# Optimization experiments

Measured on AMD Instinct MI355X. Metric: run time of the kernel, lower is better.

## Reference

```python
import jax, jax.numpy as jnp
import numpy as np

B, N_CAPS, N_VOTES, D_IN, D_H, D_CP = 1024, 64, 36, 256, 128, 32
TWO_PI = 2.0 * np.pi


def geometric_transform(pose):
    # pose: [..., 6] -> affine 3x3 matrix [..., 3, 3] (nonlinear, full affine)
    sx, sy, theta, shear, tx, ty = jnp.split(pose, 6, axis=-1)
    sx = jax.nn.sigmoid(sx) + 1e-2
    sy = jax.nn.sigmoid(sy) + 1e-2
    tx = jnp.tanh(tx * 5.0)
    ty = jnp.tanh(ty * 5.0)
    shear = jnp.tanh(shear * 5.0)
    theta = theta * TWO_PI
    c, s = jnp.cos(theta), jnp.sin(theta)
    row0 = jnp.concatenate([sx * c + shear * sy * s, -sx * s + shear * sy * c, tx], -1)
    row1 = jnp.concatenate([sy * s, sy * c, ty], -1)
    zeros = jnp.zeros_like(tx)
    row2 = jnp.concatenate([zeros, zeros, jnp.ones_like(tx)], -1)
    return jnp.stack([row0, row1, row2], axis=-2)


def setup_inputs() -> dict:
    key = jax.random.key(0)
    ks = jax.random.split(key, 16)
    u = lambda k, shp: 0.5 * (jax.random.uniform(k, shp, jnp.float32) - 0.5)
    return {
        "features": jax.random.normal(ks[0], (B, N_CAPS, D_IN), jnp.float32),
        "w1": u(ks[1], (1, N_CAPS, D_IN, D_H)),
        "b1": jnp.zeros((1, N_CAPS, 1, D_H), jnp.float32),
        "w2": u(ks[2], (1, N_CAPS, D_H, D_CP)),
        "b2": jnp.zeros((1, N_CAPS, 1, D_CP), jnp.float32),
        "caps_mlp_w": u(ks[3], (1, N_CAPS, D_CP + 1, D_H)),
        "caps_mlp_b": jnp.zeros((1, N_CAPS, 1, D_H), jnp.float32),
        "cpr_dynamic_w": u(ks[4], (1, N_CAPS, D_H, N_VOTES * 6)),
        "ccr_w": u(ks[5], (1, N_CAPS, D_H, 6)),
        "ccr_b": jnp.zeros((1, N_CAPS, 1, 6), jnp.float32),
        "pres_caps_w": u(ks[6], (1, N_CAPS, D_H, 1)),
        "pres_caps_b": jnp.zeros((1, N_CAPS, 1, 1), jnp.float32),
        "pres_vote_w": u(ks[7], (1, N_CAPS, D_H, N_VOTES)),
        "pres_vote_b": jnp.zeros((1, N_CAPS, 1, N_VOTES), jnp.float32),
        "scale_vote_w": u(ks[8], (1, N_CAPS, D_H, N_VOTES)),
        "scale_vote_b": jnp.zeros((1, N_CAPS, 1, N_VOTES), jnp.float32),
        "cpr_static": jax.random.uniform(ks[9], (1, N_CAPS, N_VOTES, 6), jnp.float32) - 0.5,
    }


def reference(features, w1, b1, w2, b2, caps_mlp_w, caps_mlp_b, cpr_dynamic_w,
              ccr_w, ccr_b, pres_caps_w, pres_caps_b, pres_vote_w, pres_vote_b,
              scale_vote_w, scale_vote_b, cpr_static):
    batch_size = features.shape[0]
    x = features[:, :, None, :]                               # [B, C, 1, 256]
    h = jax.nn.relu(x @ w1 + b1)                              # [B, C, 1, H]
    raw_caps_params = jax.nn.relu(h @ w2 + b2)                # [B, C, 1, P]
    caps_exist = jnp.ones(raw_caps_params.shape[:-1] + (1,), raw_caps_params.dtype)
    caps_params = jnp.concatenate([raw_caps_params, caps_exist], -1)  # [B, C, 1, P+1]
    caps_feat = jax.nn.relu(caps_params @ caps_mlp_w + caps_mlp_b)    # [B, C, 1, H]

    cpr_dynamic = (caps_feat @ cpr_dynamic_w).reshape(batch_size, N_CAPS, N_VOTES, 6)
    ccr = caps_feat @ ccr_w + ccr_b                           # [B, C, 1, 6]
    pres_logit_per_caps = (caps_feat @ pres_caps_w + pres_caps_b)[:, :, 0, :]   # [B, C, 1]
    pres_logit_per_vote = (caps_feat @ pres_vote_w + pres_vote_b)[:, :, 0, :]   # [B, C, V]
    scale_per_vote = (caps_feat @ scale_vote_w + scale_vote_b)[:, :, 0, :]      # [B, C, V]

    ccr_mat = geometric_transform(ccr)                        # [B, C, 1, 3, 3]
    cpr_mat = geometric_transform(cpr_dynamic + cpr_static)   # [B, C, V, 3, 3]
    votes = ccr_mat @ cpr_mat                                 # [B, C, V, 3, 3]

    pres_per_caps = jax.nn.sigmoid(pres_logit_per_caps)
    pres_per_vote = pres_per_caps * jax.nn.sigmoid(pres_logit_per_vote)
    scale_per_vote = jax.nn.softplus(scale_per_vote + 0.5) + 0.01
    dynamic_weights_l2 = jnp.sum(cpr_dynamic ** 2) / batch_size / 2.0
    return (votes, scale_per_vote, pres_per_vote, pres_logit_per_caps,
            pres_logit_per_vote, dynamic_weights_l2, raw_caps_params[:, :, 0, :], features)
```

## Files before the change

kernel.cpp:

```cpp
#include <hip/hip_runtime.h>
#include <math.h>

#define NB   1024
#define NC   64
#define DIN  256
#define DH   128
#define DCP  32
#define NV   36

#define OFF0 0
#define OFF1 21233664
#define OFF2 23592960
#define OFF3 25952256
#define OFF4 26017792
#define OFF5 28377088
#define OFF6 28377089
#define OFF7 30474241

#define SM_FST 0
#define SM_R2  4224
#define SM_R3  8576
#define SM_TOT 9664

#define SM_XS  SM_R2
#define SM_W1C (SM_R2 + 544)
#define SM_W2S SM_R2
#define SM_WM  SM_R2
#define SM_WH  SM_R2
#define SM_HD  (SM_R2 + 1280)
#define SM_HB  (SM_R2 + 3872)
#define SM_WD  SM_R2
#define SM_DYN SM_R2
#define SM_CPS SM_R3
#define SM_M   SM_R3
#define SM_PSIG (SM_R3 + 192)

__device__ __forceinline__ float sigm(float x) { return 1.0f / (1.0f + __expf(-x)); }
__device__ __forceinline__ float tanh5(float x) {
    x = fminf(fmaxf(5.0f * x, -15.0f), 15.0f);
    float z = __expf(2.0f * x);
    return (z - 1.0f) / (z + 1.0f);
}
__device__ __forceinline__ void geo(const float* p, float* m) {
    float sx = sigm(p[0]) + 0.01f;
    float sy = sigm(p[1]) + 0.01f;
    float th = p[2] * 6.28318530717958647692f;
    float sh = tanh5(p[3]);
    float tx = tanh5(p[4]);
    float ty = tanh5(p[5]);
    float cc = __cosf(th), ss = __sinf(th);
    m[0] =  sx * cc + sh * sy * ss;
    m[1] = -sx * ss + sh * sy * cc;
    m[2] = tx;
    m[3] = sy * ss;
    m[4] = sy * cc;
    m[5] = ty;
}

__global__ void zero_l2_kernel(float* out) { out[OFF5] = 0.0f; }

__global__ __launch_bounds__(256, 4)
void caps_fused_kernel(const float* __restrict__ feat,
                       const float* __restrict__ w1,  const float* __restrict__ b1,
                       const float* __restrict__ w2,  const float* __restrict__ b2,
                       const float* __restrict__ wm,  const float* __restrict__ bm,
                       const float* __restrict__ wdy,
                       const float* __restrict__ wccr,const float* __restrict__ bccr,
                       const float* __restrict__ wpc, const float* __restrict__ bpc,
                       const float* __restrict__ wpv, const float* __restrict__ bpv,
                       const float* __restrict__ wsv, const float* __restrict__ bsv,
                       const float* __restrict__ cst,
                       float* __restrict__ out)
{
    __shared__ float sm[SM_TOT];
    const int t  = threadIdx.x;
    const int c  = blockIdx.y;
    const int rb = blockIdx.x * 32;

    {
        const int tx = t & 31;
        const int ty = t >> 5;
        float acc[4][4] = {};
        const int xrow = t >> 3, xk2 = (t & 7) * 2;
        for (int k0 = 0; k0 < DIN; k0 += 16) {
            __syncthreads();
            {
                const int gi = (rb + xrow) * (NC * DIN) + c * DIN + k0 + xk2;
                const float2 v = *(const float2*)&feat[gi];
                sm[SM_XS + xrow * 17 + xk2]     = v.x;
                sm[SM_XS + xrow * 17 + xk2 + 1] = v.y;
                out[OFF7 + gi]     = v.x;
                out[OFF7 + gi + 1] = v.y;
            }
            *(float4*)&sm[SM_W1C + t * 4] =
                *(const float4*)&w1[c * (DIN * DH) + k0 * DH + t * 4];
            *(float4*)&sm[SM_W1C + (t + 256) * 4] =
                *(const float4*)&w1[c * (DIN * DH) + k0 * DH + (t + 256) * 4];
            __syncthreads();
#pragma unroll
            for (int kk = 0; kk < 16; ++kk) {
                const float a0 = sm[SM_XS + (ty * 4 + 0) * 17 + kk];
                const float a1 = sm[SM_XS + (ty * 4 + 1) * 17 + kk];
                const float a2 = sm[SM_XS + (ty * 4 + 2) * 17 + kk];
                const float a3 = sm[SM_XS + (ty * 4 + 3) * 17 + kk];
                const float4 bv = *(const float4*)&sm[SM_W1C + kk * DH + tx * 4];
                acc[0][0] += a0 * bv.x; acc[0][1] += a0 * bv.y; acc[0][2] += a0 * bv.z; acc[0][3] += a0 * bv.w;
                acc[1][0] += a1 * bv.x; acc[1][1] += a1 * bv.y; acc[1][2] += a1 * bv.z; acc[1][3] += a1 * bv.w;
                acc[2][0] += a2 * bv.x; acc[2][1] += a2 * bv.y; acc[2][2] += a2 * bv.z; acc[2][3] += a2 * bv.w;
                acc[3][0] += a3 * bv.x; acc[3][1] += a3 * bv.y; acc[3][2] += a3 * bv.z; acc[3][3] += a3 * bv.w;
            }
        }
        const float4 bb4 = *(const float4*)&b1[c * DH + tx * 4];
        const float bb[4] = { bb4.x, bb4.y, bb4.z, bb4.w };
#pragma unroll
        for (int i = 0; i < 4; ++i)
#pragma unroll
            for (int j = 0; j < 4; ++j) {
                float v = fmaxf(acc[i][j] + bb[j], 0.0f);
                sm[SM_FST + (tx * 4 + j) * 33 + (ty * 4 + i)] = v;
            }
    }
    __syncthreads();

#pragma unroll
    for (int p = 0; p < 4; ++p) {
        const int idx = t + p * 256;
        *(float4*)&sm[SM_W2S + idx * 4] = *(const float4*)&w2[c * (DH * DCP) + idx * 4];
    }
    __syncthreads();
    {
        const int b  = t & 31;
        const int j4 = (t >> 5) << 2;
        float acc[4] = {};
#pragma unroll 8
        for (int k = 0; k < DH; ++k) {
            const float h = sm[SM_FST + k * 33 + b];
            const float4 wv = *(const float4*)&sm[SM_W2S + k * DCP + j4];
            acc[0] += h * wv.x; acc[1] += h * wv.y; acc[2] += h * wv.z; acc[3] += h * wv.w;
        }
#pragma unroll
        for (int jj = 0; jj < 4; ++jj) {
            const float v = fmaxf(acc[jj] + b2[c * DCP + j4 + jj], 0.0f);
            out[OFF6 + ((rb + b) * NC + c) * DCP + j4 + jj] = v;
            sm[SM_CPS + b * 34 + j4 + jj] = v;
        }
        if (t < 32) sm[SM_CPS + t * 34 + 32] = 1.0f;
    }
    __syncthreads();

#pragma unroll
    for (int p = 0; p < 5; ++p) {
        const int idx = t + p * 256;
        if (idx < 1056)
            *(float4*)&sm[SM_WM + idx * 4] = *(const float4*)&wm[c * (33 * DH) + idx * 4];
    }
    __syncthreads();
    {
        const int b  = t & 31;
        const int nb = (t >> 5) << 4;
        float acc[16] = {};
        for (int k = 0; k < 33; ++k) {
            const float a = sm[SM_CPS + b * 34 + k];
#pragma unroll
            for (int jq = 0; jq < 4; ++jq) {
                const float4 wv = *(const float4*)&sm[SM_WM + k * DH + nb + jq * 4];
                acc[jq*4+0] += a * wv.x; acc[jq*4+1] += a * wv.y;
                acc[jq*4+2] += a * wv.z; acc[jq*4+3] += a * wv.w;
            }
        }
#pragma unroll
        for (int j = 0; j < 16; ++j) {
            const float v = fmaxf(acc[j] + bm[c * DH + nb + j], 0.0f);
            sm[SM_FST + (nb + j) * 33 + b] = v;
        }
    }
    __syncthreads();

    {
        const int txx = t & 15;
        const int tyy = t >> 4;
        float acc[2][5] = {};
        for (int k0 = 0; k0 < DH; k0 += 16) {
            __syncthreads();
#pragma unroll
            for (int p = 0; p < 5; ++p) {
                const int idx = t + p * 256;
                const int kk = idx / 80, col = idx % 80;
                const int kg = k0 + kk;
                float v = 0.0f;
                if (col < 6)        v = wccr[c * (DH * 6) + kg * 6 + col];
                else if (col == 6)  v = wpc[c * DH + kg];
                else if (col < 43)  v = wpv[c * (DH * NV) + kg * NV + (col - 7)];
                else if (col < 79)  v = wsv[c * (DH * NV) + kg * NV + (col - 43)];
                sm[SM_WH + kk * 80 + col] = v;
            }
            if (k0 == 0 && t < 80) {
                float v = 0.0f;
                if (t < 6)       v = bccr[c * 6 + t];
                else if (t == 6) v = bpc[c];
                else if (t < 43) v = bpv[c * NV + (t - 7)];
                else if (t < 79) v = bsv[c * NV + (t - 43)];
                sm[SM_HB + t] = v;
            }
            __syncthreads();
#pragma unroll
            for (int kk = 0; kk < 16; ++kk) {
                const float a0 = sm[SM_FST + (k0 + kk) * 33 + tyy * 2 + 0];
                const float a1 = sm[SM_FST + (k0 + kk) * 33 + tyy * 2 + 1];
#pragma unroll
                for (int j = 0; j < 5; ++j) {
                    const float w = sm[SM_WH + kk * 80 + txx * 5 + j];
                    acc[0][j] += a0 * w;
                    acc[1][j] += a1 * w;
                }
            }
        }
#pragma unroll
        for (int i = 0; i < 2; ++i)
#pragma unroll
            for (int j = 0; j < 5; ++j)
                sm[SM_HD + (tyy * 2 + i) * 81 + txx * 5 + j] = acc[i][j];
    }
    __syncthreads();

    if (t < 32) {
        const int b = t;
        const float plc = sm[SM_HD + b * 81 + 6] + sm[SM_HB + 6];
        out[OFF3 + (rb + b) * NC + c] = plc;
        sm[SM_PSIG + b] = sigm(plc);
        float p[6], m[6];
#pragma unroll
        for (int i = 0; i < 6; ++i) p[i] = sm[SM_HD + b * 81 + i] + sm[SM_HB + i];
        geo(p, m);
#pragma unroll
        for (int i = 0; i < 6; ++i) sm[SM_M + b * 6 + i] = m[i];
    }
    __syncthreads();

#pragma unroll
    for (int p = 0; p < 10; ++p) {
        const int item = t + p * 256;
        const int b = item / 80, col = item % 80;
        if (col >= 7 && col < 79) {
            const float v = sm[SM_HD + b * 81 + col] + sm[SM_HB + col];
            const int base = ((rb + b) * NC + c) * NV;
            if (col < 43) {
                const int o = col - 7;
                out[OFF4 + base + o] = v;
                out[OFF2 + base + o] = sm[SM_PSIG + b] * sigm(v);
            } else {
                const int o = col - 43;
                float sp = v + 0.5f;
                sp = (sp > 15.0f) ? sp : log1pf(__expf(sp));
                out[OFF1 + base + o] = sp + 0.01f;
            }
        }
    }

    float l2loc = 0.0f;
    {
        const int g   = t & 63;
        const int ty4 = t >> 6;
        float acc[8][4] = {};
        for (int k0 = 0; k0 < DH; k0 += 16) {
            __syncthreads();
#pragma unroll
            for (int p = 0; p < 7; ++p) {
                const int i2  = t + p * 256;
                const int col = (i2 * 2) % 224;
                const int row = (i2 * 2) / 224;
                float2 v = make_float2(0.0f, 0.0f);
                if (col < 216)
                    v = *(const float2*)&wdy[c * (DH * 216) + (k0 + row) * 216 + col];
                *(float2*)&sm[SM_WD + row * 224 + col] = v;
            }
            __syncthreads();
#pragma unroll
            for (int kk = 0; kk < 16; ++kk) {
                float a[8];
#pragma unroll
                for (int i = 0; i < 8; ++i)
                    a[i] = sm[SM_FST + (k0 + kk) * 33 + ty4 * 8 + i];
                const float4 w = *(const float4*)&sm[SM_WD + kk * 224 + g * 4];
#pragma unroll
                for (int i = 0; i < 8; ++i) {
                    acc[i][0] += a[i] * w.x; acc[i][1] += a[i] * w.y;
                    acc[i][2] += a[i] * w.z; acc[i][3] += a[i] * w.w;
                }
            }
        }
        for (int half = 0; half < 2; ++half) {
            __syncthreads();
            if (g < 54 && (g >= 27) == (half == 1)) {
#pragma unroll
                for (int i = 0; i < 8; ++i)
#pragma unroll
                    for (int j = 0; j < 4; ++j)
                        sm[SM_DYN + (ty4 * 8 + i) * 109 + (g * 4 + j - half * 108)] = acc[i][j];
            }
            __syncthreads();
#pragma unroll
            for (int p = 0; p < 3; ++p) {
                const int item = t + p * 256;
                if (item < 576) {
                    const int b = item / 18, vh = item % 18;
                    const int v = half * 18 + vh;
                    float dyn[6], pose[6], mB[6];
                    float ss = 0.0f;
#pragma unroll
                    for (int j = 0; j < 6; ++j) {
                        dyn[j] = sm[SM_DYN + b * 109 + vh * 6 + j];
                        ss += dyn[j] * dyn[j];
                        pose[j] = dyn[j] + cst[c * (NV * 6) + v * 6 + j];
                    }
                    l2loc += ss;
                    geo(pose, mB);
                    const float A0 = sm[SM_M + b * 6 + 0], A1 = sm[SM_M + b * 6 + 1];
                    const float A2 = sm[SM_M + b * 6 + 2], A3 = sm[SM_M + b * 6 + 3];
                    const float A4 = sm[SM_M + b * 6 + 4], A5 = sm[SM_M + b * 6 + 5];
                    const int ob = (((rb + b) * NC + c) * NV + v) * 9;
                    out[OFF0 + ob + 0] = A0 * mB[0] + A1 * mB[3];
                    out[OFF0 + ob + 1] = A0 * mB[1] + A1 * mB[4];
                    out[OFF0 + ob + 2] = A0 * mB[2] + A1 * mB[5] + A2;
                    out[OFF0 + ob + 3] = A3 * mB[0] + A4 * mB[3];
                    out[OFF0 + ob + 4] = A3 * mB[1] + A4 * mB[4];
                    out[OFF0 + ob + 5] = A3 * mB[2] + A4 * mB[5] + A5;
                    out[OFF0 + ob + 6] = 0.0f;
                    out[OFF0 + ob + 7] = 0.0f;
                    out[OFF0 + ob + 8] = 1.0f;
                }
            }
        }
    }

    l2loc += __shfl_down(l2loc, 32, 64);
    l2loc += __shfl_down(l2loc, 16, 64);
    l2loc += __shfl_down(l2loc, 8, 64);
    l2loc += __shfl_down(l2loc, 4, 64);
    l2loc += __shfl_down(l2loc, 2, 64);
    l2loc += __shfl_down(l2loc, 1, 64);
    if ((t & 63) == 0) atomicAdd(&out[OFF5], l2loc * (1.0f / 2048.0f));
}

extern "C" void kernel_launch(void* const* d_in, const int* in_sizes, int n_in,
                              void* d_out, int out_size, void* d_ws, size_t ws_size,
                              hipStream_t stream)
{
    const float* feat = (const float*)d_in[0];
    const float* w1   = (const float*)d_in[1];
    const float* b1   = (const float*)d_in[2];
    const float* w2   = (const float*)d_in[3];
    const float* b2   = (const float*)d_in[4];
    const float* wm   = (const float*)d_in[5];
    const float* bm   = (const float*)d_in[6];
    const float* wdy  = (const float*)d_in[7];
    const float* wccr = (const float*)d_in[8];
    const float* bccr = (const float*)d_in[9];
    const float* wpc  = (const float*)d_in[10];
    const float* bpc  = (const float*)d_in[11];
    const float* wpv  = (const float*)d_in[12];
    const float* bpv  = (const float*)d_in[13];
    const float* wsv  = (const float*)d_in[14];
    const float* bsv  = (const float*)d_in[15];
    const float* cst  = (const float*)d_in[16];
    float* out = (float*)d_out;

    zero_l2_kernel<<<1, 1, 0, stream>>>(out);
    dim3 grid(NB / 32, NC);
    caps_fused_kernel<<<grid, 256, 0, stream>>>(feat, w1, b1, w2, b2, wm, bm, wdy,
                                                wccr, bccr, wpc, bpc, wpv, bpv,
                                                wsv, bsv, cst, out);
}
```

Baseline: 624.8 us.

## Register-prefetch global tiles, pad shared strides for vector loads, offload feature copy

Adds register double-buffering: the next k-tile of w1/features, the w2 and wm tiles, the head weights and the wdy tiles are loaded into registers while the current tile is computed. Shared-memory row strides change from 33/34 to 36 so activations can be read as float4/float2. The constant-one column of the caps MLP is folded into a separate bias add. The features passthrough copy moves out of the kernel into a device-to-device hipMemcpyAsync. The aim is to hide global load latency and cut shared-memory instruction count. The cost is higher register pressure under launch_bounds(256,4), possible bank conflicts from the new stride, and a separate memcpy pass over the features.

```diff
diff --git a/kernel.cpp b/kernel.cpp
--- a/kernel.cpp
+++ b/kernel.cpp
@@ -18,12 +18,12 @@
 #define OFF7 30474241
 
 #define SM_FST 0
-#define SM_R2  4224
-#define SM_R3  8576
-#define SM_TOT 9664
+#define SM_R2  4608
+#define SM_R3  8960
+#define SM_TOT 10112
 
 #define SM_XS  SM_R2
-#define SM_W1C (SM_R2 + 544)
+#define SM_W1C (SM_R2 + 576)
 #define SM_W2S SM_R2
 #define SM_WM  SM_R2
 #define SM_WH  SM_R2
@@ -76,105 +76,155 @@
     const int t  = threadIdx.x;
     const int c  = blockIdx.y;
     const int rb = blockIdx.x * 32;
+    const int t4 = t * 4;
+
+    float4 w2pf[4];
 
     {
         const int tx = t & 31;
         const int ty = t >> 5;
+        const int xrow = t >> 3, xk2 = (t & 7) * 2;
+        const float* fsrc = &feat[(rb + xrow) * (NC * DIN) + c * DIN + xk2];
+        const float* w1b_ = &w1[c * (DIN * DH)];
+        float2 xr  = *(const float2*)fsrc;
+        float4 wra = *(const float4*)(w1b_ + t4);
+        float4 wrb = *(const float4*)(w1b_ + 1024 + t4);
         float acc[4][4] = {};
-        const int xrow = t >> 3, xk2 = (t & 7) * 2;
         for (int k0 = 0; k0 < DIN; k0 += 16) {
             __syncthreads();
-            {
-                const int gi = (rb + xrow) * (NC * DIN) + c * DIN + k0 + xk2;
-                const float2 v = *(const float2*)&feat[gi];
-                sm[SM_XS + xrow * 17 + xk2]     = v.x;
-                sm[SM_XS + xrow * 17 + xk2 + 1] = v.y;
-                out[OFF7 + gi]     = v.x;
-                out[OFF7 + gi + 1] = v.y;
-            }
-            *(float4*)&sm[SM_W1C + t * 4] =
-                *(const float4*)&w1[c * (DIN * DH) + k0 * DH + t * 4];
-            *(float4*)&sm[SM_W1C + (t + 256) * 4] =
-                *(const float4*)&w1[c * (DIN * DH) + k0 * DH + (t + 256) * 4];
-            __syncthreads();
+            sm[SM_XS + xk2 * 36 + xrow]       = xr.x;
+            sm[SM_XS + (xk2 + 1) * 36 + xrow] = xr.y;
+            *(float4*)&sm[SM_W1C + t4]        = wra;
+            *(float4*)&sm[SM_W1C + 1024 + t4] = wrb;
+            __syncthreads();
+            if (k0 + 16 < DIN) {
+                xr  = *(const float2*)(fsrc + k0 + 16);
+                wra = *(const float4*)(w1b_ + (k0 + 16) * DH + t4);
+                wrb = *(const float4*)(w1b_ + (k0 + 16) * DH + 1024 + t4);
+            } else {
+#pragma unroll
+                for (int p = 0; p < 4; ++p)
+                    w2pf[p] = *(const float4*)&w2[c * (DH * DCP) + (t + p * 256) * 4];
+            }
 #pragma unroll
             for (int kk = 0; kk < 16; ++kk) {
-                const float a0 = sm[SM_XS + (ty * 4 + 0) * 17 + kk];
-                const float a1 = sm[SM_XS + (ty * 4 + 1) * 17 + kk];
-                const float a2 = sm[SM_XS + (ty * 4 + 2) * 17 + kk];
-                const float a3 = sm[SM_XS + (ty * 4 + 3) * 17 + kk];
+                const float4 av = *(const float4*)&sm[SM_XS + kk * 36 + ty * 4];
                 const float4 bv = *(const float4*)&sm[SM_W1C + kk * DH + tx * 4];
-                acc[0][0] += a0 * bv.x; acc[0][1] += a0 * bv.y; acc[0][2] += a0 * bv.z; acc[0][3] += a0 * bv.w;
-                acc[1][0] += a1 * bv.x; acc[1][1] += a1 * bv.y; acc[1][2] += a1 * bv.z; acc[1][3] += a1 * bv.w;
-                acc[2][0] += a2 * bv.x; acc[2][1] += a2 * bv.y; acc[2][2] += a2 * bv.z; acc[2][3] += a2 * bv.w;
-                acc[3][0] += a3 * bv.x; acc[3][1] += a3 * bv.y; acc[3][2] += a3 * bv.z; acc[3][3] += a3 * bv.w;
-            }
-        }
-        const float4 bb4 = *(const float4*)&b1[c * DH + tx * 4];
-        const float bb[4] = { bb4.x, bb4.y, bb4.z, bb4.w };
-#pragma unroll
-        for (int i = 0; i < 4; ++i)
-#pragma unroll
-            for (int j = 0; j < 4; ++j) {
-                float v = fmaxf(acc[i][j] + bb[j], 0.0f);
-                sm[SM_FST + (tx * 4 + j) * 33 + (ty * 4 + i)] = v;
-            }
-    }
-    __syncthreads();
-
-#pragma unroll
-    for (int p = 0; p < 4; ++p) {
-        const int idx = t + p * 256;
-        *(float4*)&sm[SM_W2S + idx * 4] = *(const float4*)&w2[c * (DH * DCP) + idx * 4];
-    }
-    __syncthreads();
-    {
+                acc[0][0] += av.x * bv.x; acc[0][1] += av.x * bv.y; acc[0][2] += av.x * bv.z; acc[0][3] += av.x * bv.w;
+                acc[1][0] += av.y * bv.x; acc[1][1] += av.y * bv.y; acc[1][2] += av.y * bv.z; acc[1][3] += av.y * bv.w;
+                acc[2][0] += av.z * bv.x; acc[2][1] += av.z * bv.y; acc[2][2] += av.z * bv.z; acc[2][3] += av.z * bv.w;
+                acc[3][0] += av.w * bv.x; acc[3][1] += av.w * bv.y; acc[3][2] += av.w * bv.z; acc[3][3] += av.w * bv.w;
+            }
+        }
+        const float4 bb = *(const float4*)&b1[c * DH + tx * 4];
+        const float bbA[4] = { bb.x, bb.y, bb.z, bb.w };
+#pragma unroll
+        for (int j = 0; j < 4; ++j) {
+            float4 vv;
+            vv.x = fmaxf(acc[0][j] + bbA[j], 0.0f);
+            vv.y = fmaxf(acc[1][j] + bbA[j], 0.0f);
+            vv.z = fmaxf(acc[2][j] + bbA[j], 0.0f);
+            vv.w = fmaxf(acc[3][j] + bbA[j], 0.0f);
+            *(float4*)&sm[SM_FST + (tx * 4 + j) * 36 + ty * 4] = vv;
+        }
+    }
+
+    __syncthreads();
+#pragma unroll
+    for (int p = 0; p < 4; ++p)
+        *(float4*)&sm[SM_W2S + t4 + p * 1024] = w2pf[p];
+    __syncthreads();
+    float4 wmpf[5];
+    {
+#pragma unroll
+        for (int p = 0; p < 5; ++p) {
+            const int idx = t + p * 256;
+            if (idx < 1056)
+                wmpf[p] = *(const float4*)&wm[c * (33 * DH) + idx * 4];
+        }
         const int b  = t & 31;
         const int j4 = (t >> 5) << 2;
         float acc[4] = {};
 #pragma unroll 8
         for (int k = 0; k < DH; ++k) {
-            const float h = sm[SM_FST + k * 33 + b];
+            const float h = sm[SM_FST + k * 36 + b];
             const float4 wv = *(const float4*)&sm[SM_W2S + k * DCP + j4];
             acc[0] += h * wv.x; acc[1] += h * wv.y; acc[2] += h * wv.z; acc[3] += h * wv.w;
         }
+        const float4 b2v = *(const float4*)&b2[c * DCP + j4];
+        const float b2A[4] = { b2v.x, b2v.y, b2v.z, b2v.w };
 #pragma unroll
         for (int jj = 0; jj < 4; ++jj) {
-            const float v = fmaxf(acc[jj] + b2[c * DCP + j4 + jj], 0.0f);
+            const float v = fmaxf(acc[jj] + b2A[jj], 0.0f);
             out[OFF6 + ((rb + b) * NC + c) * DCP + j4 + jj] = v;
-            sm[SM_CPS + b * 34 + j4 + jj] = v;
-        }
-        if (t < 32) sm[SM_CPS + t * 34 + 32] = 1.0f;
-    }
-    __syncthreads();
-
+            sm[SM_CPS + b * 36 + j4 + jj] = v;
+        }
+    }
+
+    __syncthreads();
 #pragma unroll
     for (int p = 0; p < 5; ++p) {
         const int idx = t + p * 256;
         if (idx < 1056)
-            *(float4*)&sm[SM_WM + idx * 4] = *(const float4*)&wm[c * (33 * DH) + idx * 4];
-    }
-    __syncthreads();
+            *(float4*)&sm[SM_WM + idx * 4] = wmpf[p];
+    }
+    __syncthreads();
+    const float* d2p[5]; int d2adv[5]; float d2msk[5], d2pf[5];
+#pragma unroll
+    for (int p = 0; p < 5; ++p) {
+        const int idx = t + p * 256;
+        const int kp = idx / 80, colp = idx - kp * 80;
+        const float* s; int st; float mk = 1.0f;
+        if (colp < 6)       { s = &wccr[c * (DH * 6) + kp * 6 + colp];          st = 6;  }
+        else if (colp == 6) { s = &wpc [c * DH + kp];                            st = 1;  }
+        else if (colp < 43) { s = &wpv [c * (DH * NV) + kp * NV + (colp - 7)];   st = NV; }
+        else if (colp < 79) { s = &wsv [c * (DH * NV) + kp * NV + (colp - 43)];  st = NV; }
+        else                { s = &wccr[c * (DH * 6)]; st = 0; mk = 0.0f; }
+        d2pf[p]  = *s;
+        d2p[p]   = s + st * 16;
+        d2adv[p] = st * 16;
+        d2msk[p] = mk;
+    }
+    float bpf = 0.0f;
+    if (t < 80) {
+        if (t < 6)       bpf = bccr[c * 6 + t];
+        else if (t == 6) bpf = bpc[c];
+        else if (t < 43) bpf = bpv[c * NV + (t - 7)];
+        else if (t < 79) bpf = bsv[c * NV + (t - 43)];
+    }
     {
         const int b  = t & 31;
         const int nb = (t >> 5) << 4;
         float acc[16] = {};
-        for (int k = 0; k < 33; ++k) {
-            const float a = sm[SM_CPS + b * 34 + k];
-#pragma unroll
-            for (int jq = 0; jq < 4; ++jq) {
-                const float4 wv = *(const float4*)&sm[SM_WM + k * DH + nb + jq * 4];
-                acc[jq*4+0] += a * wv.x; acc[jq*4+1] += a * wv.y;
-                acc[jq*4+2] += a * wv.z; acc[jq*4+3] += a * wv.w;
-            }
-        }
-#pragma unroll
-        for (int j = 0; j < 16; ++j) {
-            const float v = fmaxf(acc[j] + bm[c * DH + nb + j], 0.0f);
-            sm[SM_FST + (nb + j) * 33 + b] = v;
-        }
-    }
-    __syncthreads();
+#pragma unroll
+        for (int k4 = 0; k4 < 8; ++k4) {
+            const float4 a4 = *(const float4*)&sm[SM_CPS + b * 36 + k4 * 4];
+            const float aA[4] = { a4.x, a4.y, a4.z, a4.w };
+#pragma unroll
+            for (int kk = 0; kk < 4; ++kk) {
+                const int k = k4 * 4 + kk;
+#pragma unroll
+                for (int jq = 0; jq < 4; ++jq) {
+                    const float4 wv = *(const float4*)&sm[SM_WM + k * DH + nb + jq * 4];
+                    acc[jq*4+0] += aA[kk] * wv.x; acc[jq*4+1] += aA[kk] * wv.y;
+                    acc[jq*4+2] += aA[kk] * wv.z; acc[jq*4+3] += aA[kk] * wv.w;
+                }
+            }
+        }
+#pragma unroll
+        for (int jq = 0; jq < 4; ++jq) {
+            const float4 wv = *(const float4*)&sm[SM_WM + 32 * DH + nb + jq * 4];
+            acc[jq*4+0] += wv.x; acc[jq*4+1] += wv.y; acc[jq*4+2] += wv.z; acc[jq*4+3] += wv.w;
+        }
+#pragma unroll
+        for (int jq = 0; jq < 4; ++jq) {
+            const float4 bmv = *(const float4*)&bm[c * DH + nb + jq * 4];
+            sm[SM_FST + (nb + jq*4 + 0) * 36 + b] = fmaxf(acc[jq*4+0] + bmv.x, 0.0f);
+            sm[SM_FST + (nb + jq*4 + 1) * 36 + b] = fmaxf(acc[jq*4+1] + bmv.y, 0.0f);
+            sm[SM_FST + (nb + jq*4 + 2) * 36 + b] = fmaxf(acc[jq*4+2] + bmv.z, 0.0f);
+            sm[SM_FST + (nb + jq*4 + 3) * 36 + b] = fmaxf(acc[jq*4+3] + bmv.w, 0.0f);
+        }
+    }
 
     {
         const int txx = t & 15;
@@ -183,35 +233,25 @@
         for (int k0 = 0; k0 < DH; k0 += 16) {
             __syncthreads();
 #pragma unroll
-            for (int p = 0; p < 5; ++p) {
-                const int idx = t + p * 256;
-                const int kk = idx / 80, col = idx % 80;
-                const int kg = k0 + kk;
-                float v = 0.0f;
-                if (col < 6)        v = wccr[c * (DH * 6) + kg * 6 + col];
-                else if (col == 6)  v = wpc[c * DH + kg];
-                else if (col < 43)  v = wpv[c * (DH * NV) + kg * NV + (col - 7)];
-                else if (col < 79)  v = wsv[c * (DH * NV) + kg * NV + (col - 43)];
-                sm[SM_WH + kk * 80 + col] = v;
-            }
-            if (k0 == 0 && t < 80) {
-                float v = 0.0f;
-                if (t < 6)       v = bccr[c * 6 + t];
-                else if (t == 6) v = bpc[c];
-                else if (t < 43) v = bpv[c * NV + (t - 7)];
-                else if (t < 79) v = bsv[c * NV + (t - 43)];
-                sm[SM_HB + t] = v;
-            }
-            __syncthreads();
+            for (int p = 0; p < 5; ++p)
+                sm[SM_WH + t + p * 256] = d2msk[p] * d2pf[p];
+            if (k0 == 0 && t < 80) sm[SM_HB + t] = bpf;
+            __syncthreads();
+            if (k0 + 16 < DH) {
+#pragma unroll
+                for (int p = 0; p < 5; ++p) {
+                    d2pf[p] = *d2p[p];
+                    d2p[p] += d2adv[p];
+                }
+            }
 #pragma unroll
             for (int kk = 0; kk < 16; ++kk) {
-                const float a0 = sm[SM_FST + (k0 + kk) * 33 + tyy * 2 + 0];
-                const float a1 = sm[SM_FST + (k0 + kk) * 33 + tyy * 2 + 1];
+                const float2 av = *(const float2*)&sm[SM_FST + (k0 + kk) * 36 + tyy * 2];
 #pragma unroll
                 for (int j = 0; j < 5; ++j) {
                     const float w = sm[SM_WH + kk * 80 + txx * 5 + j];
-                    acc[0][j] += a0 * w;
-                    acc[1][j] += a1 * w;
+                    acc[0][j] += av.x * w;
+                    acc[1][j] += av.y * w;
                 }
             }
         }
@@ -220,6 +260,25 @@
 #pragma unroll
             for (int j = 0; j < 5; ++j)
                 sm[SM_HD + (tyy * 2 + i) * 81 + txx * 5 + j] = acc[i][j];
+    }
+
+    const float* d4p[7]; int d4dst[7]; unsigned d4v = 0; float2 d4pf[7];
+    {
+        const float* wdyb = &wdy[c * (DH * 216)];
+#pragma unroll
+        for (int p = 0; p < 7; ++p) {
+            const int e2  = (t + p * 256) * 2;
+            const int row = e2 / 224, col = e2 - row * 224;
+            d4dst[p] = row * 224 + col;
+            d4pf[p]  = make_float2(0.0f, 0.0f);
+            d4p[p]   = wdyb;
+            if (col < 216) {
+                d4v |= 1u << p;
+                d4p[p]  = wdyb + row * 216 + col;
+                d4pf[p] = *(const float2*)d4p[p];
+                d4p[p] += 16 * 216;
+            }
+        }
     }
     __syncthreads();
 
@@ -228,10 +287,10 @@
         const float plc = sm[SM_HD + b * 81 + 6] + sm[SM_HB + 6];
         out[OFF3 + (rb + b) * NC + c] = plc;
         sm[SM_PSIG + b] = sigm(plc);
-        float p[6], m[6];
-#pragma unroll
-        for (int i = 0; i < 6; ++i) p[i] = sm[SM_HD + b * 81 + i] + sm[SM_HB + i];
-        geo(p, m);
+        float pp[6], m[6];
+#pragma unroll
+        for (int i = 0; i < 6; ++i) pp[i] = sm[SM_HD + b * 81 + i] + sm[SM_HB + i];
+        geo(pp, m);
 #pragma unroll
         for (int i = 0; i < 6; ++i) sm[SM_M + b * 6 + i] = m[i];
     }
@@ -265,28 +324,31 @@
         for (int k0 = 0; k0 < DH; k0 += 16) {
             __syncthreads();
 #pragma unroll
-            for (int p = 0; p < 7; ++p) {
-                const int i2  = t + p * 256;
-                const int col = (i2 * 2) % 224;
-                const int row = (i2 * 2) / 224;
-                float2 v = make_float2(0.0f, 0.0f);
-                if (col < 216)
-                    v = *(const float2*)&wdy[c * (DH * 216) + (k0 + row) * 216 + col];
-                *(float2*)&sm[SM_WD + row * 224 + col] = v;
-            }
-            __syncthreads();
+            for (int p = 0; p < 7; ++p)
+                *(float2*)&sm[SM_WD + d4dst[p]] = d4pf[p];
+            __syncthreads();
+            if (k0 + 16 < DH) {
+#pragma unroll
+                for (int p = 0; p < 7; ++p) {
+                    if ((d4v >> p) & 1) {
+                        d4pf[p] = *(const float2*)d4p[p];
+                        d4p[p] += 16 * 216;
+                    }
+                }
+            }
 #pragma unroll
             for (int kk = 0; kk < 16; ++kk) {
-                float a[8];
-#pragma unroll
-                for (int i = 0; i < 8; ++i)
-                    a[i] = sm[SM_FST + (k0 + kk) * 33 + ty4 * 8 + i];
-                const float4 w = *(const float4*)&sm[SM_WD + kk * 224 + g * 4];
-#pragma unroll
-                for (int i = 0; i < 8; ++i) {
-                    acc[i][0] += a[i] * w.x; acc[i][1] += a[i] * w.y;
-                    acc[i][2] += a[i] * w.z; acc[i][3] += a[i] * w.w;
-                }
+                const float4 a0 = *(const float4*)&sm[SM_FST + (k0 + kk) * 36 + ty4 * 8];
+                const float4 a1 = *(const float4*)&sm[SM_FST + (k0 + kk) * 36 + ty4 * 8 + 4];
+                const float4 w  = *(const float4*)&sm[SM_WD + kk * 224 + g * 4];
+                acc[0][0] += a0.x * w.x; acc[0][1] += a0.x * w.y; acc[0][2] += a0.x * w.z; acc[0][3] += a0.x * w.w;
+                acc[1][0] += a0.y * w.x; acc[1][1] += a0.y * w.y; acc[1][2] += a0.y * w.z; acc[1][3] += a0.y * w.w;
+                acc[2][0] += a0.z * w.x; acc[2][1] += a0.z * w.y; acc[2][2] += a0.z * w.z; acc[2][3] += a0.z * w.w;
+                acc[3][0] += a0.w * w.x; acc[3][1] += a0.w * w.y; acc[3][2] += a0.w * w.z; acc[3][3] += a0.w * w.w;
+                acc[4][0] += a1.x * w.x; acc[4][1] += a1.x * w.y; acc[4][2] += a1.x * w.z; acc[4][3] += a1.x * w.w;
+                acc[5][0] += a1.y * w.x; acc[5][1] += a1.y * w.y; acc[5][2] += a1.y * w.z; acc[5][3] += a1.y * w.w;
+                acc[6][0] += a1.z * w.x; acc[6][1] += a1.z * w.y; acc[6][2] += a1.z * w.z; acc[6][3] += a1.z * w.w;
+                acc[7][0] += a1.w * w.x; acc[7][1] += a1.w * w.y; acc[7][2] += a1.w * w.z; acc[7][3] += a1.w * w.w;
             }
         }
         for (int half = 0; half < 2; ++half) {
@@ -366,6 +428,9 @@
     float* out = (float*)d_out;
 
     zero_l2_kernel<<<1, 1, 0, stream>>>(out);
+    hipMemcpyAsync((void*)(out + OFF7), (const void*)feat,
+                   (size_t)NB * NC * DIN * sizeof(float),
+                   hipMemcpyDeviceToDevice, stream);
     dim3 grid(NB / 32, NC);
     caps_fused_kernel<<<grid, 256, 0, stream>>>(feat, w1, b1, w2, b2, wm, bm, wdy,
                                                 wccr, bccr, wpc, bpc, wpv, bpv,
```

Measured after the change: 653.8 us. 4.6% more time.
